# Kernel tuning notes

Measured on AMD Instinct MI355X. Metric: run time of the kernel, lower is better.

Reference implementation:

```python
import jax, jax.numpy as jnp
import numpy as np
from jax import lax

C = 256
B, H, W = 8, 64, 64


def dwconv(x, w, b, pad):
    # x: [B,C,H,W], w: [C,1,kh,kw] depthwise (groups=C), b: [C]
    y = lax.conv_general_dilated(
        x, w,
        window_strides=(1, 1),
        padding=pad,
        dimension_numbers=('NCHW', 'OIHW', 'NCHW'),
        feature_group_count=x.shape[1],
    )
    return y + b[None, :, None, None]


def setup_inputs() -> dict:
    key = jax.random.key(0)
    ks = jax.random.split(key, 16)
    s = 0.05
    inp = {
        'x': jax.random.normal(ks[0], (B, C, H, W), jnp.float32),
        'w0':   jax.random.normal(ks[1], (C, 1, 5, 5), jnp.float32) * s,
        'b0':   jax.random.normal(ks[2], (C,), jnp.float32) * s,
        'w0_1': jax.random.normal(ks[3], (C, 1, 1, 7), jnp.float32) * s,
        'b0_1': jax.random.normal(ks[4], (C,), jnp.float32) * s,
        'w0_2': jax.random.normal(ks[5], (C, 1, 7, 1), jnp.float32) * s,
        'b0_2': jax.random.normal(ks[6], (C,), jnp.float32) * s,
        'w1_1': jax.random.normal(ks[7], (C, 1, 1, 11), jnp.float32) * s,
        'b1_1': jax.random.normal(ks[8], (C,), jnp.float32) * s,
        'w1_2': jax.random.normal(ks[9], (C, 1, 11, 1), jnp.float32) * s,
        'b1_2': jax.random.normal(ks[10], (C,), jnp.float32) * s,
        'w2_1': jax.random.normal(ks[11], (C, 1, 1, 21), jnp.float32) * s,
        'b2_1': jax.random.normal(ks[12], (C,), jnp.float32) * s,
        'w2_2': jax.random.normal(ks[13], (C, 1, 21, 1), jnp.float32) * s,
        'b2_2': jax.random.normal(ks[14], (C,), jnp.float32) * s,
    }
    return inp


def reference(x, w0, b0, w0_1, b0_1, w0_2, b0_2,
              w1_1, b1_1, w1_2, b1_2, w2_1, b2_1, w2_2, b2_2):
    # 5x5 depthwise, pad 2
    attn = dwconv(x, w0, b0, ((2, 2), (2, 2)))
    # stage 0: 1x7 / 7x1 strips
    a0x = dwconv(attn, w0_1, b0_1, ((0, 0), (3, 3)))
    a0y = dwconv(attn, w0_2, b0_2, ((3, 3), (0, 0)))
    attn_0 = a0x * a0y
    # stage 1: 1x11 / 11x1 strips
    a1x = dwconv(a0x, w1_1, b1_1, ((0, 0), (5, 5)))
    a1y = dwconv(a0y, w1_2, b1_2, ((5, 5), (0, 0)))
    attn_1 = a1x * a1y
    # stage 2: 1x21 / 21x1 strips
    a2x = dwconv(a1x, w2_1, b2_1, ((0, 0), (10, 10)))
    a2y = dwconv(a1y, w2_2, b2_2, ((10, 10), (0, 0)))
    attn_2 = a2x * a2y
    return (attn_0, attn_1, attn_2)
```

## Files before the change

### kernel.cpp

```cpp
#include <hip/hip_runtime.h>


#define RA_W 4624
#define RB_W 4352
#define LDS_WORDS (RA_W + RB_W)

__device__ __forceinline__ float dppsr1(float v) {
    return __int_as_float(__builtin_amdgcn_update_dpp(
        0, __float_as_int(v), 0x111, 0xF, 0xF, false));
}
__device__ __forceinline__ float dppsr2(float v) {
    return __int_as_float(__builtin_amdgcn_update_dpp(
        0, __float_as_int(v), 0x112, 0xF, 0xF, false));
}
__device__ __forceinline__ float dppsl1(float v) {
    return __int_as_float(__builtin_amdgcn_update_dpp(
        0, __float_as_int(v), 0x101, 0xF, 0xF, false));
}
__device__ __forceinline__ float dppsl2(float v) {
    return __int_as_float(__builtin_amdgcn_update_dpp(
        0, __float_as_int(v), 0x102, 0xF, 0xF, false));
}
__device__ __forceinline__ void ld8(const float* p, float* d) {
    float4 a = *(const float4*)p, b = *(const float4*)(p + 4);
    d[0]=a.x; d[1]=a.y; d[2]=a.z; d[3]=a.w; d[4]=b.x; d[5]=b.y; d[6]=b.z; d[7]=b.w;
}
__device__ __forceinline__ void st8(float* p, const float* d) {
    float4 a, b;
    a.x=d[0]; a.y=d[1]; a.z=d[2]; a.w=d[3]; b.x=d[4]; b.y=d[5]; b.z=d[6]; b.w=d[7];
    *(float4*)p = a; *(float4*)(p + 4) = b;
}

template<int K, int W0, int N>
__device__ __forceinline__ void cpart(const float* __restrict__ wt,
                                      const float* s, float* acc) {
    #pragma unroll
    for (int v = 0; v < K; v++) {
        #pragma unroll
        for (int j = 0; j < 8; j++) {
            const int p = j + v - W0;
            if (p >= 0 && p < N) acc[j] += wt[v] * s[p];
        }
    }
}

template<int H>
__device__ __forceinline__ void sconv(const float* __restrict__ wt, float bb,
                                      const float* a, bool pm, bool np, float* acc) {
    constexpr int K = 2 * H + 1;
    float pv[H], nv[H];
    #pragma unroll
    for (int i = 0; i < H; i++) pv[i] = dppsr1(a[8 - H + i]);
    #pragma unroll
    for (int i = 0; i < H; i++) nv[i] = dppsl1(a[i]);
    #pragma unroll
    for (int i = 0; i < H; i++) pv[i] = pm ? pv[i] : 0.f;
    #pragma unroll
    for (int i = 0; i < H; i++) nv[i] = np ? nv[i] : 0.f;
    #pragma unroll
    for (int j = 0; j < 8; j++) acc[j] = bb;
    cpart<K, 0, H>(wt, pv, acc);
    cpart<K, H, 8>(wt, a, acc);
    cpart<K, H + 8, H>(wt, nv, acc);
}

__device__ __forceinline__ void sconv21(const float* __restrict__ wt, float bb,
                                        const float* a, bool pm, bool pm2,
                                        bool np, bool np2, float* acc) {
    #pragma unroll
    for (int j = 0; j < 8; j++) acc[j] = bb;
    {
        float q[2];
        q[0] = dppsr2(a[6]); q[1] = dppsr2(a[7]);
        q[0] = pm2 ? q[0] : 0.f; q[1] = pm2 ? q[1] : 0.f;
        cpart<21, 0, 2>(wt, q, acc);
    }
    {
        float pv[8];
        #pragma unroll
        for (int i = 0; i < 8; i++) pv[i] = dppsr1(a[i]);
        #pragma unroll
        for (int i = 0; i < 8; i++) pv[i] = pm ? pv[i] : 0.f;
        cpart<21, 2, 8>(wt, pv, acc);
    }
    cpart<21, 10, 8>(wt, a, acc);
    {
        float nv[8];
        #pragma unroll
        for (int i = 0; i < 8; i++) nv[i] = dppsl1(a[i]);
        #pragma unroll
        for (int i = 0; i < 8; i++) nv[i] = np ? nv[i] : 0.f;
        cpart<21, 18, 8>(wt, nv, acc);
    }
    {
        float q[2];
        q[0] = dppsl2(a[0]); q[1] = dppsl2(a[1]);
        q[0] = np2 ? q[0] : 0.f; q[1] = np2 ? q[1] : 0.f;
        cpart<21, 26, 2>(wt, q, acc);
    }
}

__global__ __launch_bounds__(512, 4)
void msca_fused(const float* __restrict__ x,
                const float* __restrict__ w0,   const float* __restrict__ b0,
                const float* __restrict__ w0_1, const float* __restrict__ b0_1,
                const float* __restrict__ w0_2, const float* __restrict__ b0_2,
                const float* __restrict__ w1_1, const float* __restrict__ b1_1,
                const float* __restrict__ w1_2, const float* __restrict__ b1_2,
                const float* __restrict__ w2_1, const float* __restrict__ b2_1,
                const float* __restrict__ w2_2, const float* __restrict__ b2_2,
                float* __restrict__ out)
{
    __shared__ __align__(16) float lds[LDS_WORDS];
    float* RA = lds;
    float* RB = lds + RA_W;

    const int t     = threadIdx.x;
    const int maj   = t >> 3;
    const int lane8 = t & 7;
    const int j0    = lane8 << 3;

    const bool pm  = lane8 >= 1, np  = lane8 <= 6;
    const bool pm2 = lane8 >= 2, np2 = lane8 <= 5;

    const int scat = maj ^ (lane8 << 3);
    const int rdb  = maj * 68 + ((lane8 ^ ((maj >> 3) & 7)) << 3);

    const int plane = blockIdx.x;
    const int ch    = plane & 255;

    const float* xg = x + (size_t)plane * 4096;
    float* o0 = out + (size_t)plane * 4096;
    float* o1 = o0 + 8388608;
    float* o2 = o1 + 8388608;

    float xr[8];
    ld8(&xg[maj * 64 + j0], xr);
    if (t < 136) { RA[t] = 0.f; RA[t + 4488] = 0.f; }
    if (t < 256) {
        int rr = 2 + (t >> 2), cc = t & 3;
        RA[rr * 68 + (cc < 2 ? cc : cc + 64)] = 0.f;
    }
    {
        float* row = &RA[(maj + 2) * 68 + j0 + 2];
        float2 p;
        p.x = xr[0]; p.y = xr[1]; ((float2*)row)[0] = p;
        p.x = xr[2]; p.y = xr[3]; ((float2*)row)[1] = p;
        p.x = xr[4]; p.y = xr[5]; ((float2*)row)[2] = p;
        p.x = xr[6]; p.y = xr[7]; ((float2*)row)[3] = p;
    }
    __syncthreads();

    float attn[8];
    {
        const float bb = b0[ch];
        #pragma unroll
        for (int j = 0; j < 8; j++) attn[j] = bb;
        const float* w0p = w0 + ch * 25;
        #pragma unroll
        for (int dr = 0; dr < 5; dr++) {
            float wnd[12];
            const float* rowp = &RA[(maj + dr) * 68 + j0];
            float4 qa = *(const float4*)rowp;
            float4 qb = *(const float4*)(rowp + 4);
            float4 qc = *(const float4*)(rowp + 8);
            wnd[0]=qa.x; wnd[1]=qa.y; wnd[2]=qa.z;  wnd[3]=qa.w;
            wnd[4]=qb.x; wnd[5]=qb.y; wnd[6]=qb.z;  wnd[7]=qb.w;
            wnd[8]=qc.x; wnd[9]=qc.y; wnd[10]=qc.z; wnd[11]=qc.w;
            #pragma unroll
            for (int v = 0; v < 5; v++) {
                const float ww = w0p[dr * 5 + v];
                #pragma unroll
                for (int j = 0; j < 8; j++) attn[j] += ww * wnd[j + v];
            }
        }
        #pragma unroll
        for (int e = 0; e < 8; e++) RB[(j0 + e) * 68 + scat] = attn[e];
    }
    __syncthreads();

    float a0x[8];
    sconv<3>(w0_1 + ch * 7, b0_1[ch], attn, pm, np, a0x);
    float stv[8];
    ld8(&RB[rdb], stv);
    float aty0[8];
    sconv<3>(w0_2 + ch * 7, b0_2[ch], stv, pm, np, aty0);
    #pragma unroll
    for (int d = 0; d < 8; d++) RA[(j0 + d) * 68 + scat] = aty0[d];
    __syncthreads();

    float prod0[8];
    {
        float y0r[8];
        ld8(&RA[rdb], y0r);
        #pragma unroll
        for (int j = 0; j < 8; j++) prod0[j] = a0x[j] * y0r[j];
    }
    float a1x[8];
    sconv<5>(w1_1 + ch * 11, b1_1[ch], a0x, pm, np, a1x);
    float aty1[8];
    sconv<5>(w1_2 + ch * 11, b1_2[ch], aty0, pm, np, aty1);
    #pragma unroll
    for (int d = 0; d < 8; d++) RB[(j0 + d) * 68 + scat] = aty1[d];
    __syncthreads();

    st8(&o0[maj * 64 + j0], prod0);
    float prod1[8];
    {
        float y1r[8];
        ld8(&RB[rdb], y1r);
        #pragma unroll
        for (int j = 0; j < 8; j++) prod1[j] = a1x[j] * y1r[j];
    }
    {
        float a2y[8];
        sconv21(w2_2 + ch * 21, b2_2[ch], aty1, pm, pm2, np, np2, a2y);
        #pragma unroll
        for (int d = 0; d < 8; d++) RA[(j0 + d) * 68 + scat] = a2y[d];
    }
    float a2x[8];
    sconv21(w2_1 + ch * 21, b2_1[ch], a1x, pm, pm2, np, np2, a2x);
    __syncthreads();

    st8(&o1[maj * 64 + j0], prod1);
    {
        float y2r[8], prod2[8];
        ld8(&RA[rdb], y2r);
        #pragma unroll
        for (int j = 0; j < 8; j++) prod2[j] = a2x[j] * y2r[j];
        st8(&o2[maj * 64 + j0], prod2);
    }
}

extern "C" void kernel_launch(void* const* d_in, const int* in_sizes, int n_in,
                              void* d_out, int out_size, void* d_ws, size_t ws_size,
                              hipStream_t stream) {
    msca_fused<<<2048, 512, 0, stream>>>(
        (const float*)d_in[0],
        (const float*)d_in[1],  (const float*)d_in[2],
        (const float*)d_in[3],  (const float*)d_in[4],
        (const float*)d_in[5],  (const float*)d_in[6],
        (const float*)d_in[7],  (const float*)d_in[8],
        (const float*)d_in[9],  (const float*)d_in[10],
        (const float*)d_in[11], (const float*)d_in[12],
        (const float*)d_in[13], (const float*)d_in[14],
        (float*)d_out);
}
```

Baseline: 42.98 us.

## Process two planes per block and prefetch the next plane's input

Each block now handles two consecutive channel planes instead of one, with half as many blocks launched. The second plane's input is loaded into registers in the middle of the first plane's compute and written into the spare LDS buffer afterwards, so its global-load latency is hidden behind work. The cost is fewer blocks for latency hiding, an extra barrier, slightly more LDS per block (RB grows to the same size as RA), and a longer serial chain of work per block.

```diff
diff --git a/kernel.cpp b/kernel.cpp
--- a/kernel.cpp
+++ b/kernel.cpp
@@ -1,9 +1,8 @@
 #include <hip/hip_runtime.h>
 
 
-#define RA_W 4624
-#define RB_W 4352
-#define LDS_WORDS (RA_W + RB_W)
+#define RG_W 4624
+#define LDS_WORDS (2 * RG_W)
 
 __device__ __forceinline__ float dppsr1(float v) {
     return __int_as_float(__builtin_amdgcn_update_dpp(
@@ -29,6 +28,21 @@
     float4 a, b;
     a.x=d[0]; a.y=d[1]; a.z=d[2]; a.w=d[3]; b.x=d[4]; b.y=d[5]; b.z=d[6]; b.w=d[7];
     *(float4*)p = a; *(float4*)(p + 4) = b;
+}
+
+__device__ __forceinline__ void commit_x(float* RX, const float* xr,
+                                         int t, int maj, int j0) {
+    if (t < 136) { RX[t] = 0.f; RX[t + 4488] = 0.f; }
+    if (t < 256) {
+        int rr = 2 + (t >> 2), cc = t & 3;
+        RX[rr * 68 + (cc < 2 ? cc : cc + 64)] = 0.f;
+    }
+    float* row = &RX[(maj + 2) * 68 + j0 + 2];
+    float2 p;
+    p.x = xr[0]; p.y = xr[1]; ((float2*)row)[0] = p;
+    p.x = xr[2]; p.y = xr[3]; ((float2*)row)[1] = p;
+    p.x = xr[4]; p.y = xr[5]; ((float2*)row)[2] = p;
+    p.x = xr[6]; p.y = xr[7]; ((float2*)row)[3] = p;
 }
 
 template<int K, int W0, int N>
@@ -113,7 +127,7 @@
 {
     __shared__ __align__(16) float lds[LDS_WORDS];
     float* RA = lds;
-    float* RB = lds + RA_W;
+    float* RB = lds + RG_W;
 
     const int t     = threadIdx.x;
     const int maj   = t >> 3;
@@ -126,116 +140,118 @@
     const int scat = maj ^ (lane8 << 3);
     const int rdb  = maj * 68 + ((lane8 ^ ((maj >> 3) & 7)) << 3);
 
-    const int plane = blockIdx.x;
-    const int ch    = plane & 255;
-
-    const float* xg = x + (size_t)plane * 4096;
-    float* o0 = out + (size_t)plane * 4096;
-    float* o1 = o0 + 8388608;
-    float* o2 = o1 + 8388608;
-
-    float xr[8];
-    ld8(&xg[maj * 64 + j0], xr);
-    if (t < 136) { RA[t] = 0.f; RA[t + 4488] = 0.f; }
-    if (t < 256) {
-        int rr = 2 + (t >> 2), cc = t & 3;
-        RA[rr * 68 + (cc < 2 ? cc : cc + 64)] = 0.f;
-    }
-    {
-        float* row = &RA[(maj + 2) * 68 + j0 + 2];
-        float2 p;
-        p.x = xr[0]; p.y = xr[1]; ((float2*)row)[0] = p;
-        p.x = xr[2]; p.y = xr[3]; ((float2*)row)[1] = p;
-        p.x = xr[4]; p.y = xr[5]; ((float2*)row)[2] = p;
-        p.x = xr[6]; p.y = xr[7]; ((float2*)row)[3] = p;
+    const int pl0 = blockIdx.x * 2;
+    const float* xg1 = x + (size_t)(pl0 + 1) * 4096;
+
+    {
+        float xr[8];
+        ld8(&x[(size_t)pl0 * 4096 + maj * 64 + j0], xr);
+        commit_x(RA, xr, t, maj, j0);
     }
     __syncthreads();
 
-    float attn[8];
-    {
-        const float bb = b0[ch];
-        #pragma unroll
-        for (int j = 0; j < 8; j++) attn[j] = bb;
-        const float* w0p = w0 + ch * 25;
-        #pragma unroll
-        for (int dr = 0; dr < 5; dr++) {
-            float wnd[12];
-            const float* rowp = &RA[(maj + dr) * 68 + j0];
-            float4 qa = *(const float4*)rowp;
-            float4 qb = *(const float4*)(rowp + 4);
-            float4 qc = *(const float4*)(rowp + 8);
-            wnd[0]=qa.x; wnd[1]=qa.y; wnd[2]=qa.z;  wnd[3]=qa.w;
-            wnd[4]=qb.x; wnd[5]=qb.y; wnd[6]=qb.z;  wnd[7]=qb.w;
-            wnd[8]=qc.x; wnd[9]=qc.y; wnd[10]=qc.z; wnd[11]=qc.w;
-            #pragma unroll
-            for (int v = 0; v < 5; v++) {
-                const float ww = w0p[dr * 5 + v];
+    float xrN[8];
+
+    #pragma unroll
+    for (int p = 0; p < 2; p++) {
+        float* RX = p ? RB : RA;
+        float* RT = p ? RA : RB;
+        const int ch = (pl0 + p) & 255;
+        float* o0 = out + (size_t)(pl0 + p) * 4096;
+        float* o1 = o0 + 8388608;
+        float* o2 = o1 + 8388608;
+
+        float attn[8];
+        {
+            const float bb = b0[ch];
+            #pragma unroll
+            for (int j = 0; j < 8; j++) attn[j] = bb;
+            const float* w0p = w0 + ch * 25;
+            #pragma unroll
+            for (int dr = 0; dr < 5; dr++) {
+                float wnd[12];
+                const float* rowp = &RX[(maj + dr) * 68 + j0];
+                float4 qa = *(const float4*)rowp;
+                float4 qb = *(const float4*)(rowp + 4);
+                float4 qc = *(const float4*)(rowp + 8);
+                wnd[0]=qa.x; wnd[1]=qa.y; wnd[2]=qa.z;  wnd[3]=qa.w;
+                wnd[4]=qb.x; wnd[5]=qb.y; wnd[6]=qb.z;  wnd[7]=qb.w;
+                wnd[8]=qc.x; wnd[9]=qc.y; wnd[10]=qc.z; wnd[11]=qc.w;
                 #pragma unroll
-                for (int j = 0; j < 8; j++) attn[j] += ww * wnd[j + v];
+                for (int v = 0; v < 5; v++) {
+                    const float ww = w0p[dr * 5 + v];
+                    #pragma unroll
+                    for (int j = 0; j < 8; j++) attn[j] += ww * wnd[j + v];
+                }
             }
-        }
-        #pragma unroll
-        for (int e = 0; e < 8; e++) RB[(j0 + e) * 68 + scat] = attn[e];
-    }
-    __syncthreads();
-
-    float a0x[8];
-    sconv<3>(w0_1 + ch * 7, b0_1[ch], attn, pm, np, a0x);
-    float stv[8];
-    ld8(&RB[rdb], stv);
-    float aty0[8];
-    sconv<3>(w0_2 + ch * 7, b0_2[ch], stv, pm, np, aty0);
-    #pragma unroll
-    for (int d = 0; d < 8; d++) RA[(j0 + d) * 68 + scat] = aty0[d];
-    __syncthreads();
-
-    float prod0[8];
-    {
-        float y0r[8];
-        ld8(&RA[rdb], y0r);
-        #pragma unroll
-        for (int j = 0; j < 8; j++) prod0[j] = a0x[j] * y0r[j];
-    }
-    float a1x[8];
-    sconv<5>(w1_1 + ch * 11, b1_1[ch], a0x, pm, np, a1x);
-    float aty1[8];
-    sconv<5>(w1_2 + ch * 11, b1_2[ch], aty0, pm, np, aty1);
-    #pragma unroll
-    for (int d = 0; d < 8; d++) RB[(j0 + d) * 68 + scat] = aty1[d];
-    __syncthreads();
-
-    st8(&o0[maj * 64 + j0], prod0);
-    float prod1[8];
-    {
-        float y1r[8];
-        ld8(&RB[rdb], y1r);
-        #pragma unroll
-        for (int j = 0; j < 8; j++) prod1[j] = a1x[j] * y1r[j];
-    }
-    {
-        float a2y[8];
-        sconv21(w2_2 + ch * 21, b2_2[ch], aty1, pm, pm2, np, np2, a2y);
-        #pragma unroll
-        for (int d = 0; d < 8; d++) RA[(j0 + d) * 68 + scat] = a2y[d];
-    }
-    float a2x[8];
-    sconv21(w2_1 + ch * 21, b2_1[ch], a1x, pm, pm2, np, np2, a2x);
-    __syncthreads();
-
-    st8(&o1[maj * 64 + j0], prod1);
-    {
-        float y2r[8], prod2[8];
-        ld8(&RA[rdb], y2r);
-        #pragma unroll
-        for (int j = 0; j < 8; j++) prod2[j] = a2x[j] * y2r[j];
-        st8(&o2[maj * 64 + j0], prod2);
+            #pragma unroll
+            for (int e = 0; e < 8; e++) RT[(j0 + e) * 68 + scat] = attn[e];
+        }
+        __syncthreads();
+
+        float a0x[8];
+        sconv<3>(w0_1 + ch * 7, b0_1[ch], attn, pm, np, a0x);
+        float stv[8];
+        ld8(&RT[rdb], stv);
+        float aty0[8];
+        sconv<3>(w0_2 + ch * 7, b0_2[ch], stv, pm, np, aty0);
+        #pragma unroll
+        for (int d = 0; d < 8; d++) RX[(j0 + d) * 68 + scat] = aty0[d];
+        __syncthreads();
+
+        float prod0[8];
+        {
+            float y0r[8];
+            ld8(&RX[rdb], y0r);
+            #pragma unroll
+            for (int j = 0; j < 8; j++) prod0[j] = a0x[j] * y0r[j];
+        }
+        float a1x[8];
+        sconv<5>(w1_1 + ch * 11, b1_1[ch], a0x, pm, np, a1x);
+        float aty1[8];
+        sconv<5>(w1_2 + ch * 11, b1_2[ch], aty0, pm, np, aty1);
+        #pragma unroll
+        for (int d = 0; d < 8; d++) RT[(j0 + d) * 68 + scat] = aty1[d];
+        __syncthreads();
+
+        st8(&o0[maj * 64 + j0], prod0);
+        if (p == 0) ld8(&xg1[maj * 64 + j0], xrN);
+        float prod1[8];
+        {
+            float y1r[8];
+            ld8(&RT[rdb], y1r);
+            #pragma unroll
+            for (int j = 0; j < 8; j++) prod1[j] = a1x[j] * y1r[j];
+        }
+        {
+            float a2y[8];
+            sconv21(w2_2 + ch * 21, b2_2[ch], aty1, pm, pm2, np, np2, a2y);
+            #pragma unroll
+            for (int d = 0; d < 8; d++) RX[(j0 + d) * 68 + scat] = a2y[d];
+        }
+        float a2x[8];
+        sconv21(w2_1 + ch * 21, b2_1[ch], a1x, pm, pm2, np, np2, a2x);
+        __syncthreads();
+
+        st8(&o1[maj * 64 + j0], prod1);
+        {
+            float y2r[8], prod2[8];
+            ld8(&RX[rdb], y2r);
+            #pragma unroll
+            for (int j = 0; j < 8; j++) prod2[j] = a2x[j] * y2r[j];
+            st8(&o2[maj * 64 + j0], prod2);
+        }
+        if (p == 0) {
+            commit_x(RT, xrN, t, maj, j0);
+            __syncthreads();
+        }
     }
 }
 
 extern "C" void kernel_launch(void* const* d_in, const int* in_sizes, int n_in,
                               void* d_out, int out_size, void* d_ws, size_t ws_size,
                               hipStream_t stream) {
-    msca_fused<<<2048, 512, 0, stream>>>(
+    msca_fused<<<1024, 512, 0, stream>>>(
         (const float*)d_in[0],
         (const float*)d_in[1],  (const float*)d_in[2],
         (const float*)d_in[3],  (const float*)d_in[4],
```

Measured after the change: 45.88 us. +6.7%, slower.

## Run vertical strip-conv chain first, then horizontal chain with one barrier

Applied to the files above, without the earlier changes.

Reorders the stages so the vertical chain (7x1, 11x1, 21x1) is computed back to back and written into three separate transposed LDS buffers. A single barrier follows, then the horizontal chain reads all three and writes the three outputs. This removes two block-wide barriers and lets independent work run without waiting. In exchange LDS use per block roughly doubles, which may cut resident blocks per CU, and attn stays live in registers longer.

```diff
diff --git a/kernel.cpp b/kernel.cpp
--- a/kernel.cpp
+++ b/kernel.cpp
@@ -1,9 +1,9 @@
 #include <hip/hip_runtime.h>
 
 
-#define RA_W 4624
-#define RB_W 4352
-#define LDS_WORDS (RA_W + RB_W)
+#define RX_W 4624
+#define RY_W 4352
+#define LDS_WORDS (RX_W + 3 * RY_W)
 
 __device__ __forceinline__ float dppsr1(float v) {
     return __int_as_float(__builtin_amdgcn_update_dpp(
@@ -112,8 +112,10 @@
                 float* __restrict__ out)
 {
     __shared__ __align__(16) float lds[LDS_WORDS];
-    float* RA = lds;
-    float* RB = lds + RA_W;
+    float* RX  = lds;
+    float* RT  = lds + RX_W;
+    float* RY1 = lds + RX_W + RY_W;
+    float* RY2 = lds + RX_W + 2 * RY_W;
 
     const int t     = threadIdx.x;
     const int maj   = t >> 3;
@@ -136,13 +138,13 @@
 
     float xr[8];
     ld8(&xg[maj * 64 + j0], xr);
-    if (t < 136) { RA[t] = 0.f; RA[t + 4488] = 0.f; }
+    if (t < 136) { RX[t] = 0.f; RX[t + 4488] = 0.f; }
     if (t < 256) {
         int rr = 2 + (t >> 2), cc = t & 3;
-        RA[rr * 68 + (cc < 2 ? cc : cc + 64)] = 0.f;
-    }
-    {
-        float* row = &RA[(maj + 2) * 68 + j0 + 2];
+        RX[rr * 68 + (cc < 2 ? cc : cc + 64)] = 0.f;
+    }
+    {
+        float* row = &RX[(maj + 2) * 68 + j0 + 2];
         float2 p;
         p.x = xr[0]; p.y = xr[1]; ((float2*)row)[0] = p;
         p.x = xr[2]; p.y = xr[3]; ((float2*)row)[1] = p;
@@ -160,7 +162,7 @@
         #pragma unroll
         for (int dr = 0; dr < 5; dr++) {
             float wnd[12];
-            const float* rowp = &RA[(maj + dr) * 68 + j0];
+            const float* rowp = &RX[(maj + dr) * 68 + j0];
             float4 qa = *(const float4*)rowp;
             float4 qb = *(const float4*)(rowp + 4);
             float4 qc = *(const float4*)(rowp + 8);
@@ -175,57 +177,51 @@
             }
         }
         #pragma unroll
-        for (int e = 0; e < 8; e++) RB[(j0 + e) * 68 + scat] = attn[e];
+        for (int e = 0; e < 8; e++) RT[(j0 + e) * 68 + scat] = attn[e];
     }
     __syncthreads();
 
-    float a0x[8];
-    sconv<3>(w0_1 + ch * 7, b0_1[ch], attn, pm, np, a0x);
-    float stv[8];
-    ld8(&RB[rdb], stv);
-    float aty0[8];
-    sconv<3>(w0_2 + ch * 7, b0_2[ch], stv, pm, np, aty0);
-    #pragma unroll
-    for (int d = 0; d < 8; d++) RA[(j0 + d) * 68 + scat] = aty0[d];
+    {
+        float stv[8];
+        ld8(&RT[rdb], stv);
+        float a0y[8];
+        sconv<3>(w0_2 + ch * 7, b0_2[ch], stv, pm, np, a0y);
+        #pragma unroll
+        for (int d = 0; d < 8; d++) RX[(j0 + d) * 68 + scat] = a0y[d];
+        float a1y[8];
+        sconv<5>(w1_2 + ch * 11, b1_2[ch], a0y, pm, np, a1y);
+        #pragma unroll
+        for (int d = 0; d < 8; d++) RY1[(j0 + d) * 68 + scat] = a1y[d];
+        float a2y[8];
+        sconv21(w2_2 + ch * 21, b2_2[ch], a1y, pm, pm2, np, np2, a2y);
+        #pragma unroll
+        for (int d = 0; d < 8; d++) RY2[(j0 + d) * 68 + scat] = a2y[d];
+    }
     __syncthreads();
 
-    float prod0[8];
-    {
-        float y0r[8];
-        ld8(&RA[rdb], y0r);
+    {
+        float y0r[8], y1r[8], y2r[8];
+        ld8(&RX[rdb],  y0r);
+        ld8(&RY1[rdb], y1r);
+        ld8(&RY2[rdb], y2r);
+
+        float a0x[8];
+        sconv<3>(w0_1 + ch * 7, b0_1[ch], attn, pm, np, a0x);
+        float prod0[8];
         #pragma unroll
         for (int j = 0; j < 8; j++) prod0[j] = a0x[j] * y0r[j];
-    }
-    float a1x[8];
-    sconv<5>(w1_1 + ch * 11, b1_1[ch], a0x, pm, np, a1x);
-    float aty1[8];
-    sconv<5>(w1_2 + ch * 11, b1_2[ch], aty0, pm, np, aty1);
-    #pragma unroll
-    for (int d = 0; d < 8; d++) RB[(j0 + d) * 68 + scat] = aty1[d];
-    __syncthreads();
-
-    st8(&o0[maj * 64 + j0], prod0);
-    float prod1[8];
-    {
-        float y1r[8];
-        ld8(&RB[rdb], y1r);
+        st8(&o0[maj * 64 + j0], prod0);
+
+        float a1x[8];
+        sconv<5>(w1_1 + ch * 11, b1_1[ch], a0x, pm, np, a1x);
+        float prod1[8];
         #pragma unroll
         for (int j = 0; j < 8; j++) prod1[j] = a1x[j] * y1r[j];
-    }
-    {
-        float a2y[8];
-        sconv21(w2_2 + ch * 21, b2_2[ch], aty1, pm, pm2, np, np2, a2y);
-        #pragma unroll
-        for (int d = 0; d < 8; d++) RA[(j0 + d) * 68 + scat] = a2y[d];
-    }
-    float a2x[8];
-    sconv21(w2_1 + ch * 21, b2_1[ch], a1x, pm, pm2, np, np2, a2x);
-    __syncthreads();
-
-    st8(&o1[maj * 64 + j0], prod1);
-    {
-        float y2r[8], prod2[8];
-        ld8(&RA[rdb], y2r);
+        st8(&o1[maj * 64 + j0], prod1);
+
+        float a2x[8];
+        sconv21(w2_1 + ch * 21, b2_1[ch], a1x, pm, pm2, np, np2, a2x);
+        float prod2[8];
         #pragma unroll
         for (int j = 0; j < 8; j++) prod2[j] = a2x[j] * y2r[j];
         st8(&o2[maj * 64 + j0], prod2);
```

Result: no change. 43.42 us (+1.0%).
